# Performance work log

Measured on AMD Instinct MI355X. Metric: run time of the kernel, lower is better.

The kernel has to match this reference:

```python
import jax, jax.numpy as jnp
import numpy as np

N = 50000   # nodes
E = 800000  # edges (avg degree 16)
D = 96      # input feature dim
U = 96      # units (== D, so no dense_i projection)


def _glorot(key, fan_in, fan_out):
    limit = np.sqrt(6.0 / (fan_in + fan_out)).astype(np.float32)
    return jax.random.uniform(key, (fan_in, fan_out), jnp.float32, -limit, limit)


def setup_inputs() -> dict:
    key = jax.random.key(0)
    ks = jax.random.split(key, 8)
    X = jax.random.normal(ks[0], (N, D), jnp.float32)
    row = jax.random.randint(ks[1], (E,), 0, N, jnp.int32)   # destination nodes
    col = jax.random.randint(ks[2], (E,), 0, N, jnp.int32)   # source nodes
    a_vals = jax.random.uniform(ks[3], (E,), jnp.float32)    # adjacency values
    return {
        "X": X,
        "a_vals": a_vals,
        "Wn": _glorot(ks[4], D, U), "bn": jnp.zeros((U,), jnp.float32),
        "Wgi": _glorot(ks[5], D, U), "bgi": jnp.zeros((U,), jnp.float32),
        "Wgn": _glorot(ks[6], U, U), "bgn": jnp.zeros((U,), jnp.float32),
        "row": row, "col": col,
    }


def reference(X, a_vals, Wn, bn, Wgi, bgi, Wgn, bgn, row, col):
    # new_X = dense_n(X); new_X = A @ new_X  (SpMM via gather + segment_sum)
    newX = X @ Wn + bn                       # [N, U]
    msgs = a_vals[:, None] * newX[col]       # [E, U]
    agg = jax.ops.segment_sum(msgs, row, num_segments=N)  # [N, U]
    # gate = sigmoid(dense_gate_i(X) + dense_gate_n(agg))
    gate = jax.nn.sigmoid(X @ Wgi + bgi + agg @ Wgn + bgn)
    # units == inp_dim -> no dense_i; gated residual combine
    return agg * gate + X * (1.0 - gate)
```

## Files before the change

kernel.cpp:

```cpp
#include <hip/hip_runtime.h>
#include <math.h>


#define DU 96
#define DU4 24
#define CAP 64

typedef unsigned int uint;
typedef unsigned short ushort;
typedef __attribute__((ext_vector_type(8))) short short8;
typedef __attribute__((ext_vector_type(4))) float f32x4;

__device__ inline uint bf16r(float x) {
  uint u = __float_as_uint(x);
  return (u + 0x7FFFu + ((u >> 16) & 1u)) >> 16;
}

__global__ __launch_bounds__(256) void k_fuse1(
    const float* __restrict__ X, const float* __restrict__ Wn,
    const float* __restrict__ bn, const float* __restrict__ Wgi,
    const float* __restrict__ Wgn, const int* __restrict__ row,
    const int* __restrict__ col, const float* __restrict__ a_vals,
    ushort* __restrict__ Xb, ushort* __restrict__ newXb,
    ushort* __restrict__ WTgi, ushort* __restrict__ WTgn,
    int* __restrict__ cnt, int2* __restrict__ epad, int N, int E, int ntile) {
  __shared__ ushort WL[9216];
  __shared__ ushort Xs[64][104];
  const int tid = threadIdx.x;
  const int lane = tid & 63, w = tid >> 6;
  const int m = lane & 15, q = lane >> 4;

  if ((int)blockIdx.x < ntile) {
    if (blockIdx.x == 0) {
      for (int i = tid; i < DU * DU; i += 256) {
        int n = i / DU, k = i % DU;
        WTgi[i] = (ushort)bf16r(Wgi[k * DU + n]);
      }
    } else if (blockIdx.x == 1) {
      for (int i = tid; i < DU * DU; i += 256) {
        int n = i / DU, k = i % DU;
        WTgn[i] = (ushort)bf16r(Wgn[k * DU + n]);
      }
    }
    for (int idx = tid; idx < 9216; idx += 256) {
      int j = idx & 7, ln = (idx >> 3) & 63, tk = idx >> 9;
      int ks = tk / 6, t = tk % 6;
      int k = ks * 32 + (ln >> 4) * 8 + j;
      int n = t * 16 + (ln & 15);
      WL[idx] = (ushort)bf16r(Wn[k * DU + n]);
    }
    const int row0 = blockIdx.x * 64;
    for (int i = tid; i < 64 * 48; i += 256) {
      int r = i / 48, cu = i % 48;
      int gr = row0 + r;
      uint packed = 0;
      if (gr < N) {
        float2 v = ((const float2*)X)[(size_t)gr * 48 + cu];
        packed = bf16r(v.x) | (bf16r(v.y) << 16);
        ((uint*)Xb)[(size_t)gr * 48 + cu] = packed;
      }
      *(uint*)&Xs[r][cu * 2] = packed;
    }
    __syncthreads();

    f32x4 acc[6];
#pragma unroll
    for (int t = 0; t < 6; ++t) acc[t] = (f32x4){0.f, 0.f, 0.f, 0.f};
#pragma unroll
    for (int ks = 0; ks < 3; ++ks) {
      short8 af = *(const short8*)&Xs[w * 16 + m][ks * 32 + q * 8];
#pragma unroll
      for (int t = 0; t < 6; ++t) {
        short8 bf = *(const short8*)&WL[((ks * 6 + t) * 64 + lane) * 8];
        acc[t] = __builtin_amdgcn_mfma_f32_16x16x32_bf16(af, bf, acc[t], 0, 0, 0);
      }
    }
    __syncthreads();
#pragma unroll
    for (int t = 0; t < 6; ++t) {
      int c = t * 16 + m;
      float bb = bn[c];
#pragma unroll
      for (int i = 0; i < 4; ++i)
        Xs[w * 16 + q * 4 + i][c] = (ushort)bf16r(acc[t][i] + bb);
    }
    __syncthreads();
    for (int i = tid; i < 64 * 48; i += 256) {
      int r = i / 48, cu = i % 48;
      int gr = row0 + r;
      if (gr < N) ((uint*)newXb)[(size_t)gr * 48 + cu] = *(uint*)&Xs[r][cu * 2];
    }
  }

  {
    const int g = blockIdx.x & 7;
    const int sub = blockIdx.x >> 3;
    const int nsub = gridDim.x >> 3;
    const int d0 = (int)((long long)N * g >> 3);
    const int d1 = (int)((long long)N * (g + 1) >> 3);
    for (int i = sub * 256 + tid; i < E; i += nsub * 256) {
      int d = row[i];
      if (d >= d0 && d < d1) {
        int slot = atomicAdd(&cnt[d], 1);
        epad[(size_t)d * CAP + slot] = make_int2(col[i], __float_as_int(a_vals[i]));
      }
    }
  }
}

__global__ __launch_bounds__(256) void k_agg(const ushort* __restrict__ newXb,
                                             const int* __restrict__ cnt,
                                             const int2* __restrict__ epad,
                                             ushort* __restrict__ aggb, int N) {
  int i = blockIdx.x * 256 + threadIdx.x;
  int r = i / DU4;
  int c = i % DU4;
  if (r >= N) return;
  int e1 = cnt[r];
  const int2* ep = epad + (size_t)r * CAP;
  float4 accA = make_float4(0.f, 0.f, 0.f, 0.f);
  float4 accB = make_float4(0.f, 0.f, 0.f, 0.f);
  int e = 0;
  for (; e + 4 <= e1; e += 4) {
    int2 p0 = ep[e + 0];
    int2 p1 = ep[e + 1];
    int2 p2 = ep[e + 2];
    int2 p3 = ep[e + 3];
    uint2 v0 = *(const uint2*)(newXb + (size_t)p0.x * DU + c * 4);
    uint2 v1 = *(const uint2*)(newXb + (size_t)p1.x * DU + c * 4);
    uint2 v2 = *(const uint2*)(newXb + (size_t)p2.x * DU + c * 4);
    uint2 v3 = *(const uint2*)(newXb + (size_t)p3.x * DU + c * 4);
    float a0 = __int_as_float(p0.y), a1 = __int_as_float(p1.y);
    float a2 = __int_as_float(p2.y), a3 = __int_as_float(p3.y);
    accA.x = fmaf(a0, __uint_as_float(v0.x << 16), accA.x);
    accA.y = fmaf(a0, __uint_as_float(v0.x & 0xFFFF0000u), accA.y);
    accA.z = fmaf(a0, __uint_as_float(v0.y << 16), accA.z);
    accA.w = fmaf(a0, __uint_as_float(v0.y & 0xFFFF0000u), accA.w);
    accB.x = fmaf(a1, __uint_as_float(v1.x << 16), accB.x);
    accB.y = fmaf(a1, __uint_as_float(v1.x & 0xFFFF0000u), accB.y);
    accB.z = fmaf(a1, __uint_as_float(v1.y << 16), accB.z);
    accB.w = fmaf(a1, __uint_as_float(v1.y & 0xFFFF0000u), accB.w);
    accA.x = fmaf(a2, __uint_as_float(v2.x << 16), accA.x);
    accA.y = fmaf(a2, __uint_as_float(v2.x & 0xFFFF0000u), accA.y);
    accA.z = fmaf(a2, __uint_as_float(v2.y << 16), accA.z);
    accA.w = fmaf(a2, __uint_as_float(v2.y & 0xFFFF0000u), accA.w);
    accB.x = fmaf(a3, __uint_as_float(v3.x << 16), accB.x);
    accB.y = fmaf(a3, __uint_as_float(v3.x & 0xFFFF0000u), accB.y);
    accB.z = fmaf(a3, __uint_as_float(v3.y << 16), accB.z);
    accB.w = fmaf(a3, __uint_as_float(v3.y & 0xFFFF0000u), accB.w);
  }
  for (; e < e1; ++e) {
    int2 p = ep[e];
    float a = __int_as_float(p.y);
    uint2 v = *(const uint2*)(newXb + (size_t)p.x * DU + c * 4);
    accA.x = fmaf(a, __uint_as_float(v.x << 16), accA.x);
    accA.y = fmaf(a, __uint_as_float(v.x & 0xFFFF0000u), accA.y);
    accA.z = fmaf(a, __uint_as_float(v.y << 16), accA.z);
    accA.w = fmaf(a, __uint_as_float(v.y & 0xFFFF0000u), accA.w);
  }
  accA.x += accB.x; accA.y += accB.y; accA.z += accB.z; accA.w += accB.w;
  uint2 o;
  o.x = bf16r(accA.x) | (bf16r(accA.y) << 16);
  o.y = bf16r(accA.z) | (bf16r(accA.w) << 16);
  ((uint2*)aggb)[(size_t)r * DU4 + c] = o;
}

__global__ __launch_bounds__(256) void k_gateM(const ushort* __restrict__ Xb,
                                               const ushort* __restrict__ aggb,
                                               const ushort* __restrict__ WTgi,
                                               const ushort* __restrict__ WTgn,
                                               const float* __restrict__ bgi,
                                               const float* __restrict__ bgn,
                                               const float* __restrict__ X,
                                               float* __restrict__ Out, int N) {
  __shared__ float Gs[64][100];
  const int tid = threadIdx.x;
  const int lane = tid & 63, w = tid >> 6;
  const int m = lane & 15, q = lane >> 4;
  const int row0 = blockIdx.x * 64;
  int ar = row0 + w * 16 + m;
  if (ar > N - 1) ar = N - 1;

  f32x4 acc[6];
#pragma unroll
  for (int t = 0; t < 6; ++t) acc[t] = (f32x4){0.f, 0.f, 0.f, 0.f};

#pragma unroll
  for (int ks = 0; ks < 3; ++ks) {
    short8 af = *(const short8*)(Xb + (size_t)ar * DU + ks * 32 + q * 8);
#pragma unroll
    for (int t = 0; t < 6; ++t) {
      short8 bf = *(const short8*)(WTgi + (size_t)(t * 16 + m) * DU + ks * 32 + q * 8);
      acc[t] = __builtin_amdgcn_mfma_f32_16x16x32_bf16(af, bf, acc[t], 0, 0, 0);
    }
  }
#pragma unroll
  for (int ks = 0; ks < 3; ++ks) {
    short8 af = *(const short8*)(aggb + (size_t)ar * DU + ks * 32 + q * 8);
#pragma unroll
    for (int t = 0; t < 6; ++t) {
      short8 bf = *(const short8*)(WTgn + (size_t)(t * 16 + m) * DU + ks * 32 + q * 8);
      acc[t] = __builtin_amdgcn_mfma_f32_16x16x32_bf16(af, bf, acc[t], 0, 0, 0);
    }
  }

#pragma unroll
  for (int t = 0; t < 6; ++t) {
    int c = t * 16 + m;
    float bb = bgi[c] + bgn[c];
#pragma unroll
    for (int i = 0; i < 4; ++i) {
      float z = acc[t][i] + bb;
      Gs[w * 16 + q * 4 + i][c] = 1.f / (1.f + __expf(-z));
    }
  }
  __syncthreads();

  for (int j = tid; j < 64 * DU4; j += 256) {
    int r = j / DU4, c = j % DU4;
    int gr = row0 + r;
    if (gr < N) {
      float4 xv = ((const float4*)X)[(size_t)gr * DU4 + c];
      uint2 av = ((const uint2*)aggb)[(size_t)gr * DU4 + c];
      float a0 = __uint_as_float(av.x << 16);
      float a1 = __uint_as_float(av.x & 0xFFFF0000u);
      float a2 = __uint_as_float(av.y << 16);
      float a3 = __uint_as_float(av.y & 0xFFFF0000u);
      const float* gp = &Gs[r][c * 4];
      float4 o;
      o.x = xv.x + gp[0] * (a0 - xv.x);
      o.y = xv.y + gp[1] * (a1 - xv.y);
      o.z = xv.z + gp[2] * (a2 - xv.z);
      o.w = xv.w + gp[3] * (a3 - xv.w);
      ((float4*)Out)[(size_t)gr * DU4 + c] = o;
    }
  }
}

extern "C" void kernel_launch(void* const* d_in, const int* in_sizes, int n_in,
                              void* d_out, int out_size, void* d_ws, size_t ws_size,
                              hipStream_t stream) {
  const float* X      = (const float*)d_in[0];
  const float* a_vals = (const float*)d_in[1];
  const float* Wn     = (const float*)d_in[2];
  const float* bn     = (const float*)d_in[3];
  const float* Wgi    = (const float*)d_in[4];
  const float* bgi    = (const float*)d_in[5];
  const float* Wgn    = (const float*)d_in[6];
  const float* bgn    = (const float*)d_in[7];
  const int*   row    = (const int*)d_in[8];
  const int*   col    = (const int*)d_in[9];
  float* out = (float*)d_out;

  const int N = in_sizes[0] / DU;
  const int E = in_sizes[1];
  const int ntile = (N + 63) / 64;
  const int G1 = ((ntile + 7) / 8) * 8;

  int2*   epad  = (int2*)d_ws;
  ushort* Xb    = (ushort*)(epad + (size_t)N * CAP + CAP);
  ushort* newXb = Xb + (size_t)N * DU;
  ushort* aggb  = newXb + (size_t)N * DU;
  ushort* WTgi  = aggb + (size_t)N * DU;
  ushort* WTgn  = WTgi + DU * DU;
  int*    cnt   = (int*)(WTgn + DU * DU);

  hipMemsetAsync(cnt, 0, (size_t)N * sizeof(int), stream);

  k_fuse1<<<G1, 256, 0, stream>>>(X, Wn, bn, Wgi, Wgn, row, col, a_vals,
                                  Xb, newXb, WTgi, WTgn, cnt, epad, N, E, ntile);
  k_agg  <<<((size_t)N * DU4 + 255) / 256, 256, 0, stream>>>(newXb, cnt, epad, aggb, N);
  k_gateM<<<ntile, 256, 0, stream>>>(Xb, aggb, WTgi, WTgn, bgi, bgn, X, out, N);
}
```

Baseline: 192.7 us.

## Replicate edge buckets per block group and widen aggregation loads to 16 bytes

Edge bucketing now uses 8 per-group copies of the count and padded edge arrays. Each block inserts every edge it reads into its group's copy, so the old scheme where each group rescanned all edges and filtered by destination range is gone, and atomic contention is spread out. The aggregation kernel sums the 8 copies and has each thread handle 8 bf16 columns with uint4 loads, halving the thread count. This enlarges the workspace and the memset, makes aggregation walk 8 small bucket lists per row, and silently drops edges if any group's per-node bucket exceeds 32.

```diff
diff --git a/kernel.cpp b/kernel.cpp
--- a/kernel.cpp
+++ b/kernel.cpp
@@ -4,7 +4,8 @@
 
 #define DU 96
 #define DU4 24
-#define CAP 64
+#define NCH 12
+#define CAP 32
 
 typedef unsigned int uint;
 typedef unsigned short ushort;
@@ -23,7 +24,7 @@
     const int* __restrict__ col, const float* __restrict__ a_vals,
     ushort* __restrict__ Xb, ushort* __restrict__ newXb,
     ushort* __restrict__ WTgi, ushort* __restrict__ WTgn,
-    int* __restrict__ cnt, int2* __restrict__ epad, int N, int E, int ntile) {
+    int* __restrict__ cnt8, int2* __restrict__ epad8, int N, int E, int ntile) {
   __shared__ ushort WL[9216];
   __shared__ ushort Xs[64][104];
   const int tid = threadIdx.x;
@@ -94,75 +95,78 @@
 
   {
     const int g = blockIdx.x & 7;
-    const int sub = blockIdx.x >> 3;
-    const int nsub = gridDim.x >> 3;
-    const int d0 = (int)((long long)N * g >> 3);
-    const int d1 = (int)((long long)N * (g + 1) >> 3);
-    for (int i = sub * 256 + tid; i < E; i += nsub * 256) {
+    int* cnt = cnt8 + (size_t)g * N;
+    int2* ep = epad8 + (size_t)g * N * CAP;
+    for (int i = blockIdx.x * 256 + tid; i < E; i += gridDim.x * 256) {
       int d = row[i];
-      if (d >= d0 && d < d1) {
-        int slot = atomicAdd(&cnt[d], 1);
-        epad[(size_t)d * CAP + slot] = make_int2(col[i], __float_as_int(a_vals[i]));
-      }
+      int slot = atomicAdd(&cnt[d], 1);
+      if (slot < CAP)
+        ep[(size_t)d * CAP + slot] = make_int2(col[i], __float_as_int(a_vals[i]));
     }
   }
 }
 
 __global__ __launch_bounds__(256) void k_agg(const ushort* __restrict__ newXb,
-                                             const int* __restrict__ cnt,
-                                             const int2* __restrict__ epad,
+                                             const int* __restrict__ cnt8,
+                                             const int2* __restrict__ epad8,
                                              ushort* __restrict__ aggb, int N) {
   int i = blockIdx.x * 256 + threadIdx.x;
-  int r = i / DU4;
-  int c = i % DU4;
+  int r = i / NCH;
+  int c = i % NCH;
   if (r >= N) return;
-  int e1 = cnt[r];
-  const int2* ep = epad + (size_t)r * CAP;
-  float4 accA = make_float4(0.f, 0.f, 0.f, 0.f);
-  float4 accB = make_float4(0.f, 0.f, 0.f, 0.f);
-  int e = 0;
-  for (; e + 4 <= e1; e += 4) {
-    int2 p0 = ep[e + 0];
-    int2 p1 = ep[e + 1];
-    int2 p2 = ep[e + 2];
-    int2 p3 = ep[e + 3];
-    uint2 v0 = *(const uint2*)(newXb + (size_t)p0.x * DU + c * 4);
-    uint2 v1 = *(const uint2*)(newXb + (size_t)p1.x * DU + c * 4);
-    uint2 v2 = *(const uint2*)(newXb + (size_t)p2.x * DU + c * 4);
-    uint2 v3 = *(const uint2*)(newXb + (size_t)p3.x * DU + c * 4);
-    float a0 = __int_as_float(p0.y), a1 = __int_as_float(p1.y);
-    float a2 = __int_as_float(p2.y), a3 = __int_as_float(p3.y);
-    accA.x = fmaf(a0, __uint_as_float(v0.x << 16), accA.x);
-    accA.y = fmaf(a0, __uint_as_float(v0.x & 0xFFFF0000u), accA.y);
-    accA.z = fmaf(a0, __uint_as_float(v0.y << 16), accA.z);
-    accA.w = fmaf(a0, __uint_as_float(v0.y & 0xFFFF0000u), accA.w);
-    accB.x = fmaf(a1, __uint_as_float(v1.x << 16), accB.x);
-    accB.y = fmaf(a1, __uint_as_float(v1.x & 0xFFFF0000u), accB.y);
-    accB.z = fmaf(a1, __uint_as_float(v1.y << 16), accB.z);
-    accB.w = fmaf(a1, __uint_as_float(v1.y & 0xFFFF0000u), accB.w);
-    accA.x = fmaf(a2, __uint_as_float(v2.x << 16), accA.x);
-    accA.y = fmaf(a2, __uint_as_float(v2.x & 0xFFFF0000u), accA.y);
-    accA.z = fmaf(a2, __uint_as_float(v2.y << 16), accA.z);
-    accA.w = fmaf(a2, __uint_as_float(v2.y & 0xFFFF0000u), accA.w);
-    accB.x = fmaf(a3, __uint_as_float(v3.x << 16), accB.x);
-    accB.y = fmaf(a3, __uint_as_float(v3.x & 0xFFFF0000u), accB.y);
-    accB.z = fmaf(a3, __uint_as_float(v3.y << 16), accB.z);
-    accB.w = fmaf(a3, __uint_as_float(v3.y & 0xFFFF0000u), accB.w);
-  }
-  for (; e < e1; ++e) {
-    int2 p = ep[e];
-    float a = __int_as_float(p.y);
-    uint2 v = *(const uint2*)(newXb + (size_t)p.x * DU + c * 4);
-    accA.x = fmaf(a, __uint_as_float(v.x << 16), accA.x);
-    accA.y = fmaf(a, __uint_as_float(v.x & 0xFFFF0000u), accA.y);
-    accA.z = fmaf(a, __uint_as_float(v.y << 16), accA.z);
-    accA.w = fmaf(a, __uint_as_float(v.y & 0xFFFF0000u), accA.w);
-  }
-  accA.x += accB.x; accA.y += accB.y; accA.z += accB.z; accA.w += accB.w;
-  uint2 o;
-  o.x = bf16r(accA.x) | (bf16r(accA.y) << 16);
-  o.y = bf16r(accA.z) | (bf16r(accA.w) << 16);
-  ((uint2*)aggb)[(size_t)r * DU4 + c] = o;
+  float acc[8];
+#pragma unroll
+  for (int j = 0; j < 8; ++j) acc[j] = 0.f;
+
+#pragma unroll
+  for (int g = 0; g < 8; ++g) {
+    int e1 = cnt8[(size_t)g * N + r];
+    if (e1 > CAP) e1 = CAP;
+    const int2* ep = epad8 + ((size_t)g * N + r) * CAP;
+    int e = 0;
+    for (; e + 2 <= e1; e += 2) {
+      int2 p0 = ep[e + 0];
+      int2 p1 = ep[e + 1];
+      uint4 v0 = *(const uint4*)(newXb + (size_t)p0.x * DU + c * 8);
+      uint4 v1 = *(const uint4*)(newXb + (size_t)p1.x * DU + c * 8);
+      float a0 = __int_as_float(p0.y), a1 = __int_as_float(p1.y);
+      acc[0] = fmaf(a0, __uint_as_float(v0.x << 16), acc[0]);
+      acc[1] = fmaf(a0, __uint_as_float(v0.x & 0xFFFF0000u), acc[1]);
+      acc[2] = fmaf(a0, __uint_as_float(v0.y << 16), acc[2]);
+      acc[3] = fmaf(a0, __uint_as_float(v0.y & 0xFFFF0000u), acc[3]);
+      acc[4] = fmaf(a0, __uint_as_float(v0.z << 16), acc[4]);
+      acc[5] = fmaf(a0, __uint_as_float(v0.z & 0xFFFF0000u), acc[5]);
+      acc[6] = fmaf(a0, __uint_as_float(v0.w << 16), acc[6]);
+      acc[7] = fmaf(a0, __uint_as_float(v0.w & 0xFFFF0000u), acc[7]);
+      acc[0] = fmaf(a1, __uint_as_float(v1.x << 16), acc[0]);
+      acc[1] = fmaf(a1, __uint_as_float(v1.x & 0xFFFF0000u), acc[1]);
+      acc[2] = fmaf(a1, __uint_as_float(v1.y << 16), acc[2]);
+      acc[3] = fmaf(a1, __uint_as_float(v1.y & 0xFFFF0000u), acc[3]);
+      acc[4] = fmaf(a1, __uint_as_float(v1.z << 16), acc[4]);
+      acc[5] = fmaf(a1, __uint_as_float(v1.z & 0xFFFF0000u), acc[5]);
+      acc[6] = fmaf(a1, __uint_as_float(v1.w << 16), acc[6]);
+      acc[7] = fmaf(a1, __uint_as_float(v1.w & 0xFFFF0000u), acc[7]);
+    }
+    if (e < e1) {
+      int2 p = ep[e];
+      uint4 v = *(const uint4*)(newXb + (size_t)p.x * DU + c * 8);
+      float a = __int_as_float(p.y);
+      acc[0] = fmaf(a, __uint_as_float(v.x << 16), acc[0]);
+      acc[1] = fmaf(a, __uint_as_float(v.x & 0xFFFF0000u), acc[1]);
+      acc[2] = fmaf(a, __uint_as_float(v.y << 16), acc[2]);
+      acc[3] = fmaf(a, __uint_as_float(v.y & 0xFFFF0000u), acc[3]);
+      acc[4] = fmaf(a, __uint_as_float(v.z << 16), acc[4]);
+      acc[5] = fmaf(a, __uint_as_float(v.z & 0xFFFF0000u), acc[5]);
+      acc[6] = fmaf(a, __uint_as_float(v.w << 16), acc[6]);
+      acc[7] = fmaf(a, __uint_as_float(v.w & 0xFFFF0000u), acc[7]);
+    }
+  }
+  uint4 o;
+  o.x = bf16r(acc[0]) | (bf16r(acc[1]) << 16);
+  o.y = bf16r(acc[2]) | (bf16r(acc[3]) << 16);
+  o.z = bf16r(acc[4]) | (bf16r(acc[5]) << 16);
+  o.w = bf16r(acc[6]) | (bf16r(acc[7]) << 16);
+  *(uint4*)(aggb + (size_t)r * DU + c * 8) = o;
 }
 
 __global__ __launch_bounds__(256) void k_gateM(const ushort* __restrict__ Xb,
@@ -257,18 +261,18 @@
   const int ntile = (N + 63) / 64;
   const int G1 = ((ntile + 7) / 8) * 8;
 
-  int2*   epad  = (int2*)d_ws;
-  ushort* Xb    = (ushort*)(epad + (size_t)N * CAP + CAP);
+  int2*   epad8 = (int2*)d_ws;
+  ushort* Xb    = (ushort*)(epad8 + (size_t)8 * N * CAP);
   ushort* newXb = Xb + (size_t)N * DU;
   ushort* aggb  = newXb + (size_t)N * DU;
   ushort* WTgi  = aggb + (size_t)N * DU;
   ushort* WTgn  = WTgi + DU * DU;
-  int*    cnt   = (int*)(WTgn + DU * DU);
-
-  hipMemsetAsync(cnt, 0, (size_t)N * sizeof(int), stream);
+  int*    cnt8  = (int*)(WTgn + DU * DU);
+
+  hipMemsetAsync(cnt8, 0, (size_t)8 * N * sizeof(int), stream);
 
   k_fuse1<<<G1, 256, 0, stream>>>(X, Wn, bn, Wgi, Wgn, row, col, a_vals,
-                                  Xb, newXb, WTgi, WTgn, cnt, epad, N, E, ntile);
-  k_agg  <<<((size_t)N * DU4 + 255) / 256, 256, 0, stream>>>(newXb, cnt, epad, aggb, N);
+                                  Xb, newXb, WTgi, WTgn, cnt8, epad8, N, E, ntile);
+  k_agg  <<<((size_t)N * NCH + 255) / 256, 256, 0, stream>>>(newXb, cnt8, epad8, aggb, N);
   k_gateM<<<ntile, 256, 0, stream>>>(Xb, aggb, WTgi, WTgn, bgi, bgn, X, out, N);
 }
```

Result: slower. 224.4 us (+16.5%).

## Fuse SpMM aggregation into gate kernel via shared-memory agg tile

Applied to the files above, without the earlier changes.

Merges the aggregation kernel into the gate/MFMA kernel: each 64-row block gathers neighbor features for its rows into an LDS bf16 tile, then uses it for the MFMA gate GEMM and the residual combine. This removes the global write and reread of the bf16 agg buffer and one kernel launch. The epad writes also become nontemporal stores, and edge counts are clamped to CAP. The cost is fewer threads doing the gather (782 blocks of 256, each thread handling 6 row-chunks), which lowers the memory-level parallelism available to hide gather latency.

```diff
diff --git a/kernel.cpp b/kernel.cpp
--- a/kernel.cpp
+++ b/kernel.cpp
@@ -102,84 +102,88 @@
       int d = row[i];
       if (d >= d0 && d < d1) {
         int slot = atomicAdd(&cnt[d], 1);
-        epad[(size_t)d * CAP + slot] = make_int2(col[i], __float_as_int(a_vals[i]));
-      }
-    }
-  }
-}
-
-__global__ __launch_bounds__(256) void k_agg(const ushort* __restrict__ newXb,
-                                             const int* __restrict__ cnt,
-                                             const int2* __restrict__ epad,
-                                             ushort* __restrict__ aggb, int N) {
-  int i = blockIdx.x * 256 + threadIdx.x;
-  int r = i / DU4;
-  int c = i % DU4;
-  if (r >= N) return;
-  int e1 = cnt[r];
-  const int2* ep = epad + (size_t)r * CAP;
-  float4 accA = make_float4(0.f, 0.f, 0.f, 0.f);
-  float4 accB = make_float4(0.f, 0.f, 0.f, 0.f);
-  int e = 0;
-  for (; e + 4 <= e1; e += 4) {
-    int2 p0 = ep[e + 0];
-    int2 p1 = ep[e + 1];
-    int2 p2 = ep[e + 2];
-    int2 p3 = ep[e + 3];
-    uint2 v0 = *(const uint2*)(newXb + (size_t)p0.x * DU + c * 4);
-    uint2 v1 = *(const uint2*)(newXb + (size_t)p1.x * DU + c * 4);
-    uint2 v2 = *(const uint2*)(newXb + (size_t)p2.x * DU + c * 4);
-    uint2 v3 = *(const uint2*)(newXb + (size_t)p3.x * DU + c * 4);
-    float a0 = __int_as_float(p0.y), a1 = __int_as_float(p1.y);
-    float a2 = __int_as_float(p2.y), a3 = __int_as_float(p3.y);
-    accA.x = fmaf(a0, __uint_as_float(v0.x << 16), accA.x);
-    accA.y = fmaf(a0, __uint_as_float(v0.x & 0xFFFF0000u), accA.y);
-    accA.z = fmaf(a0, __uint_as_float(v0.y << 16), accA.z);
-    accA.w = fmaf(a0, __uint_as_float(v0.y & 0xFFFF0000u), accA.w);
-    accB.x = fmaf(a1, __uint_as_float(v1.x << 16), accB.x);
-    accB.y = fmaf(a1, __uint_as_float(v1.x & 0xFFFF0000u), accB.y);
-    accB.z = fmaf(a1, __uint_as_float(v1.y << 16), accB.z);
-    accB.w = fmaf(a1, __uint_as_float(v1.y & 0xFFFF0000u), accB.w);
-    accA.x = fmaf(a2, __uint_as_float(v2.x << 16), accA.x);
-    accA.y = fmaf(a2, __uint_as_float(v2.x & 0xFFFF0000u), accA.y);
-    accA.z = fmaf(a2, __uint_as_float(v2.y << 16), accA.z);
-    accA.w = fmaf(a2, __uint_as_float(v2.y & 0xFFFF0000u), accA.w);
-    accB.x = fmaf(a3, __uint_as_float(v3.x << 16), accB.x);
-    accB.y = fmaf(a3, __uint_as_float(v3.x & 0xFFFF0000u), accB.y);
-    accB.z = fmaf(a3, __uint_as_float(v3.y << 16), accB.z);
-    accB.w = fmaf(a3, __uint_as_float(v3.y & 0xFFFF0000u), accB.w);
-  }
-  for (; e < e1; ++e) {
-    int2 p = ep[e];
-    float a = __int_as_float(p.y);
-    uint2 v = *(const uint2*)(newXb + (size_t)p.x * DU + c * 4);
-    accA.x = fmaf(a, __uint_as_float(v.x << 16), accA.x);
-    accA.y = fmaf(a, __uint_as_float(v.x & 0xFFFF0000u), accA.y);
-    accA.z = fmaf(a, __uint_as_float(v.y << 16), accA.z);
-    accA.w = fmaf(a, __uint_as_float(v.y & 0xFFFF0000u), accA.w);
-  }
-  accA.x += accB.x; accA.y += accB.y; accA.z += accB.z; accA.w += accB.w;
-  uint2 o;
-  o.x = bf16r(accA.x) | (bf16r(accA.y) << 16);
-  o.y = bf16r(accA.z) | (bf16r(accA.w) << 16);
-  ((uint2*)aggb)[(size_t)r * DU4 + c] = o;
-}
-
-__global__ __launch_bounds__(256) void k_gateM(const ushort* __restrict__ Xb,
-                                               const ushort* __restrict__ aggb,
-                                               const ushort* __restrict__ WTgi,
-                                               const ushort* __restrict__ WTgn,
-                                               const float* __restrict__ bgi,
-                                               const float* __restrict__ bgn,
-                                               const float* __restrict__ X,
-                                               float* __restrict__ Out, int N) {
+        long long pv = (long long)(uint)col[i] |
+                       ((long long)(uint)__float_as_uint(a_vals[i]) << 32);
+        __builtin_nontemporal_store(pv, (long long*)&epad[(size_t)d * CAP + slot]);
+      }
+    }
+  }
+}
+
+__global__ __launch_bounds__(256) void k_aggGate(
+    const ushort* __restrict__ Xb, const ushort* __restrict__ newXb,
+    const int* __restrict__ cnt, const int2* __restrict__ epad,
+    const ushort* __restrict__ WTgi, const ushort* __restrict__ WTgn,
+    const float* __restrict__ bgi, const float* __restrict__ bgn,
+    const float* __restrict__ X, float* __restrict__ Out, int N) {
+  __shared__ ushort As[64][104];
   __shared__ float Gs[64][100];
   const int tid = threadIdx.x;
   const int lane = tid & 63, w = tid >> 6;
   const int m = lane & 15, q = lane >> 4;
   const int row0 = blockIdx.x * 64;
+
+#pragma unroll
+  for (int p = 0; p < 6; ++p) {
+    int j = p * 256 + tid;
+    int lr = j / DU4, c = j % DU4;
+    int r = row0 + lr;
+    float4 accA = make_float4(0.f, 0.f, 0.f, 0.f);
+    float4 accB = make_float4(0.f, 0.f, 0.f, 0.f);
+    if (r < N) {
+      int e1 = cnt[r];
+      if (e1 > CAP) e1 = CAP;
+      const int2* ep = epad + (size_t)r * CAP;
+      int e = 0;
+      for (; e + 4 <= e1; e += 4) {
+        int2 p0 = ep[e + 0];
+        int2 p1 = ep[e + 1];
+        int2 p2 = ep[e + 2];
+        int2 p3 = ep[e + 3];
+        uint2 v0 = *(const uint2*)(newXb + (size_t)p0.x * DU + c * 4);
+        uint2 v1 = *(const uint2*)(newXb + (size_t)p1.x * DU + c * 4);
+        uint2 v2 = *(const uint2*)(newXb + (size_t)p2.x * DU + c * 4);
+        uint2 v3 = *(const uint2*)(newXb + (size_t)p3.x * DU + c * 4);
+        float a0 = __int_as_float(p0.y), a1 = __int_as_float(p1.y);
+        float a2 = __int_as_float(p2.y), a3 = __int_as_float(p3.y);
+        accA.x = fmaf(a0, __uint_as_float(v0.x << 16), accA.x);
+        accA.y = fmaf(a0, __uint_as_float(v0.x & 0xFFFF0000u), accA.y);
+        accA.z = fmaf(a0, __uint_as_float(v0.y << 16), accA.z);
+        accA.w = fmaf(a0, __uint_as_float(v0.y & 0xFFFF0000u), accA.w);
+        accB.x = fmaf(a1, __uint_as_float(v1.x << 16), accB.x);
+        accB.y = fmaf(a1, __uint_as_float(v1.x & 0xFFFF0000u), accB.y);
+        accB.z = fmaf(a1, __uint_as_float(v1.y << 16), accB.z);
+        accB.w = fmaf(a1, __uint_as_float(v1.y & 0xFFFF0000u), accB.w);
+        accA.x = fmaf(a2, __uint_as_float(v2.x << 16), accA.x);
+        accA.y = fmaf(a2, __uint_as_float(v2.x & 0xFFFF0000u), accA.y);
+        accA.z = fmaf(a2, __uint_as_float(v2.y << 16), accA.z);
+        accA.w = fmaf(a2, __uint_as_float(v2.y & 0xFFFF0000u), accA.w);
+        accB.x = fmaf(a3, __uint_as_float(v3.x << 16), accB.x);
+        accB.y = fmaf(a3, __uint_as_float(v3.x & 0xFFFF0000u), accB.y);
+        accB.z = fmaf(a3, __uint_as_float(v3.y << 16), accB.z);
+        accB.w = fmaf(a3, __uint_as_float(v3.y & 0xFFFF0000u), accB.w);
+      }
+      for (; e < e1; ++e) {
+        int2 pp = ep[e];
+        float a = __int_as_float(pp.y);
+        uint2 v = *(const uint2*)(newXb + (size_t)pp.x * DU + c * 4);
+        accA.x = fmaf(a, __uint_as_float(v.x << 16), accA.x);
+        accA.y = fmaf(a, __uint_as_float(v.x & 0xFFFF0000u), accA.y);
+        accA.z = fmaf(a, __uint_as_float(v.y << 16), accA.z);
+        accA.w = fmaf(a, __uint_as_float(v.y & 0xFFFF0000u), accA.w);
+      }
+      accA.x += accB.x; accA.y += accB.y; accA.z += accB.z; accA.w += accB.w;
+    }
+    uint2 o;
+    o.x = bf16r(accA.x) | (bf16r(accA.y) << 16);
+    o.y = bf16r(accA.z) | (bf16r(accA.w) << 16);
+    *(uint2*)&As[lr][c * 4] = o;
+  }
+  __syncthreads();
+
   int ar = row0 + w * 16 + m;
   if (ar > N - 1) ar = N - 1;
+  const int lr = w * 16 + m;
 
   f32x4 acc[6];
 #pragma unroll
@@ -196,7 +200,7 @@
   }
 #pragma unroll
   for (int ks = 0; ks < 3; ++ks) {
-    short8 af = *(const short8*)(aggb + (size_t)ar * DU + ks * 32 + q * 8);
+    short8 af = *(const short8*)&As[lr][ks * 32 + q * 8];
 #pragma unroll
     for (int t = 0; t < 6; ++t) {
       short8 bf = *(const short8*)(WTgn + (size_t)(t * 16 + m) * DU + ks * 32 + q * 8);
@@ -221,7 +225,7 @@
     int gr = row0 + r;
     if (gr < N) {
       float4 xv = ((const float4*)X)[(size_t)gr * DU4 + c];
-      uint2 av = ((const uint2*)aggb)[(size_t)gr * DU4 + c];
+      uint2 av = *(const uint2*)&As[r][c * 4];
       float a0 = __uint_as_float(av.x << 16);
       float a1 = __uint_as_float(av.x & 0xFFFF0000u);
       float a2 = __uint_as_float(av.y << 16);
@@ -260,8 +264,7 @@
   int2*   epad  = (int2*)d_ws;
   ushort* Xb    = (ushort*)(epad + (size_t)N * CAP + CAP);
   ushort* newXb = Xb + (size_t)N * DU;
-  ushort* aggb  = newXb + (size_t)N * DU;
-  ushort* WTgi  = aggb + (size_t)N * DU;
+  ushort* WTgi  = newXb + (size_t)N * DU;
   ushort* WTgn  = WTgi + DU * DU;
   int*    cnt   = (int*)(WTgn + DU * DU);
 
@@ -269,6 +272,6 @@
 
   k_fuse1<<<G1, 256, 0, stream>>>(X, Wn, bn, Wgi, Wgn, row, col, a_vals,
                                   Xb, newXb, WTgi, WTgn, cnt, epad, N, E, ntile);
-  k_agg  <<<((size_t)N * DU4 + 255) / 256, 256, 0, stream>>>(newXb, cnt, epad, aggb, N);
-  k_gateM<<<ntile, 256, 0, stream>>>(Xb, aggb, WTgi, WTgn, bgi, bgn, X, out, N);
-}
+  k_aggGate<<<ntile, 256, 0, stream>>>(Xb, newXb, cnt, epad, WTgi, WTgn,
+                                       bgi, bgn, X, out, N);
+}
```

Result: slower. 197.8 us (+2.7%).
